# Optimization experiments

Hardware: AMD Instinct MI355X
Metric: run time of the kernel (lower is better)

Reference implementation:

```python
import jax, jax.numpy as jnp
import numpy as np

H = 32          # num attention heads
KVH = 8         # num kv heads
D = 64          # head dim
HID = 2048      # hidden size
MAXB = 1024     # max_bias_length
BASE = 10000.0  # rope theta


def _rope(x, pos):
    # x: (B, S, h, D), pos: (S,) -- GPT-NeoX half-split rotary
    half = D // 2
    inv_freq = 1.0 / (BASE ** (jnp.arange(0, D, 2, dtype=jnp.float32) / D))  # (half,)
    ang = pos[:, None].astype(jnp.float32) * inv_freq                         # (S, half)
    cos = jnp.cos(ang)[None, :, None, :]
    sin = jnp.sin(ang)[None, :, None, :]
    x1, x2 = x[..., :half], x[..., half:]
    return jnp.concatenate([x1 * cos - x2 * sin, x2 * cos + x1 * sin], axis=-1)


def setup_inputs() -> dict:
    key = jax.random.key(0)
    ks = jax.random.split(key, 7)
    B, S = 2, 1024
    hidden_states = jax.random.normal(ks[0], (B, S, HID), dtype=jnp.float32)
    attention_mask = jnp.broadcast_to(
        jnp.tril(jnp.ones((S, S), dtype=jnp.int32))[None, None], (B, 1, S, S))
    # weights stored as (in, out): y = x @ W  (same math as torch Linear)
    Wq = jax.random.normal(ks[1], (HID, H * D), dtype=jnp.float32) * 0.02
    Wk = jax.random.normal(ks[2], (HID, KVH * D), dtype=jnp.float32) * 0.02
    Wv = jax.random.normal(ks[3], (HID, KVH * D), dtype=jnp.float32) * 0.02
    Wo = jax.random.normal(ks[4], (H * D, HID), dtype=jnp.float32) * 0.02
    bias_diag = jax.random.normal(ks[5], (H, MAXB), dtype=jnp.float32) * 0.001
    softmax_offset = jnp.zeros((H,), dtype=jnp.float32)
    return {"hidden_states": hidden_states, "attention_mask": attention_mask,
            "Wq": Wq, "Wk": Wk, "Wv": Wv, "Wo": Wo,
            "bias_diag": bias_diag, "softmax_offset": softmax_offset}


def reference(hidden_states, attention_mask, Wq, Wk, Wv, Wo, bias_diag, softmax_offset):
    B, S, _ = hidden_states.shape
    scaling = D ** (-0.5)
    pos = jnp.arange(S)

    q = (hidden_states @ Wq).reshape(B, S, H, D)
    k = (hidden_states @ Wk).reshape(B, S, KVH, D)
    v = (hidden_states @ Wv).reshape(B, S, KVH, D)

    q = _rope(q, pos)
    k = _rope(k, pos)

    # (B, H, S, D); repeat_kv via repeat on head axis
    q = q.transpose(0, 2, 1, 3)
    k = jnp.repeat(k.transpose(0, 2, 1, 3), H // KVH, axis=1)
    v = jnp.repeat(v.transpose(0, 2, 1, 3), H // KVH, axis=1)

    scores = jnp.einsum('bhqd,bhkd->bhqk', q, k) * scaling

    # learnable diagonal relative-position bias
    rel = pos[:, None] - pos[None, :]                     # (S, S)
    valid = ((rel >= 0) & (rel < MAXB)).astype(scores.dtype)
    idx = jnp.clip(rel, 0, MAXB - 1)
    bias = bias_diag[:, idx] * valid                      # (H, S, S)
    scores = scores + bias[None]

    scores = jnp.where(attention_mask[:, :, :, :S] == 0, -jnp.inf, scores)

    weights = jax.nn.softmax(scores.astype(jnp.float32), axis=-1)

    # adaptive offset subtraction + relu
    offset = jnp.abs(softmax_offset + 1.0)[None, :, None, None]
    num_visible = (pos + 1).astype(jnp.float32)[None, None, :, None]  # along query dim
    weights = jax.nn.relu(weights - offset / num_visible)

    attn_out = jnp.einsum('bhqk,bhkd->bhqd', weights.astype(v.dtype), v)
    attn_out = attn_out.transpose(0, 2, 1, 3).reshape(B, S, H * D)
    return attn_out @ Wo
```

## Files before the change

### kernel.cpp

```cpp
#include <hip/hip_runtime.h>
#include <cstdint>
#include <cstddef>

#define BB   2
#define SS   1024
#define HID  2048
#define HH   32
#define KVHH 8
#define DD   64
#define NQKV 3072
#define QKW  2560

typedef __attribute__((ext_vector_type(8))) short bf16x8;
typedef __attribute__((ext_vector_type(4))) float f32x4;
typedef __attribute__((ext_vector_type(4))) unsigned int u32x4;

__device__ __forceinline__ unsigned short f2bf(float f) {
    unsigned int u = __float_as_uint(f);
    unsigned int r = (u + 0x7fffu + ((u >> 16) & 1u)) >> 16;
    return (unsigned short)r;
}

__device__ __forceinline__ void g2l16(const unsigned short* g, unsigned short* l) {
    __builtin_amdgcn_global_load_lds(
        (__attribute__((address_space(1))) void*)(unsigned short*)g,
        (__attribute__((address_space(3))) void*)l,
        16, 0, 0);
}

__global__ __launch_bounds__(256) void prep(
    const float* __restrict__ hidden,
    const float* __restrict__ Wq, const float* __restrict__ Wk,
    const float* __restrict__ Wv, const float* __restrict__ Wo,
    unsigned short* __restrict__ hidden_bf,
    unsigned short* __restrict__ WqkvT,
    unsigned short* __restrict__ WoT)
{
    const int z   = blockIdx.z;
    const int tid = threadIdx.x;

    if (z == 4) {
        int r0 = blockIdx.y * 64, c0 = blockIdx.x * 64;
        #pragma unroll
        for (int p = 0; p < 4; ++p) {
            int f = tid + p * 256;
            int row = r0 + (f >> 4), c4 = c0 + (f & 15) * 4;
            float4 v = *(const float4*)&hidden[(size_t)row * 2048 + c4];
            ushort4 o;
            o.x = f2bf(v.x); o.y = f2bf(v.y); o.z = f2bf(v.z); o.w = f2bf(v.w);
            *(ushort4*)&hidden_bf[(size_t)row * 2048 + c4] = o;
        }
        return;
    }

    const float* W;
    unsigned short* Wt;
    int N;
    if (z == 0)      { W = Wq; Wt = WqkvT;                        N = 2048; }
    else if (z == 1) { W = Wk; Wt = WqkvT + (size_t)2048 * 2048;  N = 512;  }
    else if (z == 2) { W = Wv; Wt = WqkvT + (size_t)2560 * 2048;  N = 512;  }
    else             { W = Wo; Wt = WoT;                          N = 2048; }
    if (blockIdx.x * 64 >= N) return;

    __shared__ float t[64][68];
    const int n0 = blockIdx.x * 64, k0 = blockIdx.y * 64;
    #pragma unroll
    for (int p = 0; p < 4; ++p) {
        int f = tid + p * 256;
        int row = f >> 4, c4 = (f & 15) * 4;
        float4 v = *(const float4*)&W[(size_t)(k0 + row) * N + n0 + c4];
        t[row][c4 + 0] = v.x; t[row][c4 + 1] = v.y;
        t[row][c4 + 2] = v.z; t[row][c4 + 3] = v.w;
    }
    __syncthreads();
    #pragma unroll
    for (int p = 0; p < 4; ++p) {
        int f = tid + p * 256;
        int nrow = f >> 4, kc4 = (f & 15) * 4;
        ushort4 o;
        o.x = f2bf(t[kc4 + 0][nrow]);
        o.y = f2bf(t[kc4 + 1][nrow]);
        o.z = f2bf(t[kc4 + 2][nrow]);
        o.w = f2bf(t[kc4 + 3][nrow]);
        *(ushort4*)&Wt[(size_t)(n0 + nrow) * 2048 + k0 + kc4] = o;
    }
}

__global__ __launch_bounds__(256) void gemm_qkv_fused(
    const unsigned short* __restrict__ A,
    const unsigned short* __restrict__ Bt,
    unsigned short* __restrict__ qk_bf,
    unsigned short* __restrict__ v_t)
{
    __shared__ __align__(16) char smem[33024];
    short* Asb = (short*)smem;
    short* Bsb = (short*)(smem + 16384);
    float* Ctf = (float*)smem;

    const int tid  = threadIdx.x;
    const int lane = tid & 63;
    const int wave = tid >> 6;
    const int quad = lane >> 4;
    const int l15  = lane & 15;
    const int wm = (wave >> 1) * 64, wn = (wave & 1) * 64;
    const int m0 = blockIdx.y * 128, n0 = blockIdx.x * 128;
    const int K = 2048;

    f32x4 acc[4][4] = {};

    for (int k0 = 0; k0 < K; k0 += 64) {
        #pragma unroll
        for (int p = 0; p < 4; ++p) {
            int ci = tid + p * 256;
            int row = ci >> 3, sc = (ci & 7) ^ (row & 7);
            g2l16(&A[(size_t)(m0 + row) * K + k0 + sc * 8],
                  (unsigned short*)Asb + ci * 8);
        }
        #pragma unroll
        for (int p = 0; p < 4; ++p) {
            int ci = tid + p * 256;
            int row = ci >> 3, sc = (ci & 7) ^ (row & 7);
            g2l16(&Bt[(size_t)(n0 + row) * K + k0 + sc * 8],
                  (unsigned short*)Bsb + ci * 8);
        }
        __syncthreads();

        #pragma unroll
        for (int s = 0; s < 2; ++s) {
            bf16x8 af[4], bfr[4];
            #pragma unroll
            for (int i = 0; i < 4; ++i) {
                int row = wm + i * 16 + l15;
                af[i] = *(const bf16x8*)(Asb + row * 64 +
                        ((((s << 2) | quad) ^ (row & 7)) * 8));
            }
            #pragma unroll
            for (int j = 0; j < 4; ++j) {
                int row = wn + j * 16 + l15;
                bfr[j] = *(const bf16x8*)(Bsb + row * 64 +
                        ((((s << 2) | quad) ^ (row & 7)) * 8));
            }
            #pragma unroll
            for (int i = 0; i < 4; ++i)
                #pragma unroll
                for (int j = 0; j < 4; ++j)
                    acc[i][j] = __builtin_amdgcn_mfma_f32_16x16x32_bf16(
                        af[i], bfr[j], acc[i][j], 0, 0, 0);
        }
        __syncthreads();
    }

    const int bx = blockIdx.x;
    const int b  = m0 >> 10;
    const int s0 = m0 & 1023;
    const int hcg = bx * 128;

    #pragma unroll 1
    for (int ph = 0; ph < 2; ++ph) {
        if (ph) __syncthreads();
        if ((wave >> 1) == ph) {
            #pragma unroll
            for (int i = 0; i < 4; ++i)
                #pragma unroll
                for (int j = 0; j < 4; ++j)
                    #pragma unroll
                    for (int rg = 0; rg < 4; ++rg)
                        Ctf[(i * 16 + quad * 4 + rg) * 129 + wn + j * 16 + l15]
                            = acc[i][j][rg];
        }
        __syncthreads();

        if (bx < 20) {
            const float scale = (bx < 16) ? 0.125f : 1.0f;
            #pragma unroll
            for (int p = 0; p < 4; ++p) {
                int idx = tid + p * 256;
                int row = idx >> 4, hi = (idx >> 3) & 1, t0 = (idx & 7) * 4;
                int s = s0 + ph * 64 + row;
                ushort4 o1, o2;
                #pragma unroll
                for (int k = 0; k < 4; ++k) {
                    int t = t0 + k;
                    float x1 = Ctf[row * 129 + hi * 64 + t];
                    float x2 = Ctf[row * 129 + hi * 64 + t + 32];
                    float inv = __expf(-(float)t * 0.28782313662425572f);
                    float ang = (float)s * inv;
                    float c  = __cosf(ang);
                    float sn = __sinf(ang);
                    ((unsigned short*)&o1)[k] = f2bf((x1 * c - x2 * sn) * scale);
                    ((unsigned short*)&o2)[k] = f2bf((x2 * c + x1 * sn) * scale);
                }
                unsigned short* dst =
                    qk_bf + (size_t)(m0 + ph * 64 + row) * QKW + hcg + hi * 64;
                *(ushort4*)&dst[t0]      = o1;
                *(ushort4*)&dst[t0 + 32] = o2;
            }
        } else {
            const int vb = b * 512 + (bx - 20) * 128;
            #pragma unroll
            for (int p = 0; p < 8; ++p) {
                int idx = tid + p * 256;
                int cc = idx >> 4, srow = (idx & 15) * 4;
                ushort4 o;
                #pragma unroll
                for (int k = 0; k < 4; ++k)
                    ((unsigned short*)&o)[k] = f2bf(Ctf[(srow + k) * 129 + cc]);
                *(ushort4*)&v_t[(size_t)(vb + cc) * 1024 + s0 + ph * 64 + srow] = o;
            }
        }
    }
}

__global__ __launch_bounds__(256) void gemm_bf16_bt(
    const unsigned short* __restrict__ A,
    const unsigned short* __restrict__ Bt,
    float* __restrict__ C, int M, int N, int K)
{
    __shared__ short Asb[128 * 64];
    __shared__ short Bsb[64 * 64];

    const int tid  = threadIdx.x;
    const int lane = tid & 63;
    const int wave = tid >> 6;
    const int quad = lane >> 4;
    const int l15  = lane & 15;
    const int wm = (wave >> 1) * 64, wn = (wave & 1) * 32;
    const int m0 = blockIdx.y * 128, n0 = blockIdx.x * 64;

    f32x4 acc[4][2] = {};

    for (int k0 = 0; k0 < K; k0 += 64) {
        #pragma unroll
        for (int p = 0; p < 4; ++p) {
            int ci = tid + p * 256;
            int row = ci >> 3, sc = (ci & 7) ^ (row & 7);
            g2l16(&A[(size_t)(m0 + row) * K + k0 + sc * 8],
                  (unsigned short*)Asb + ci * 8);
        }
        #pragma unroll
        for (int p = 0; p < 2; ++p) {
            int ci = tid + p * 256;
            int row = ci >> 3, sc = (ci & 7) ^ (row & 7);
            g2l16(&Bt[(size_t)(n0 + row) * K + k0 + sc * 8],
                  (unsigned short*)Bsb + ci * 8);
        }
        __syncthreads();

        #pragma unroll
        for (int s = 0; s < 2; ++s) {
            bf16x8 af[4], bfr[2];
            #pragma unroll
            for (int i = 0; i < 4; ++i) {
                int row = wm + i * 16 + l15;
                af[i] = *(const bf16x8*)(Asb + row * 64 +
                        ((((s << 2) | quad) ^ (row & 7)) * 8));
            }
            #pragma unroll
            for (int j = 0; j < 2; ++j) {
                int row = wn + j * 16 + l15;
                bfr[j] = *(const bf16x8*)(Bsb + row * 64 +
                        ((((s << 2) | quad) ^ (row & 7)) * 8));
            }
            #pragma unroll
            for (int i = 0; i < 4; ++i)
                #pragma unroll
                for (int j = 0; j < 2; ++j)
                    acc[i][j] = __builtin_amdgcn_mfma_f32_16x16x32_bf16(
                        af[i], bfr[j], acc[i][j], 0, 0, 0);
        }
        __syncthreads();
    }

    #pragma unroll
    for (int i = 0; i < 4; ++i) {
        int grow = m0 + wm + i * 16 + quad * 4;
        #pragma unroll
        for (int j = 0; j < 2; ++j) {
            int gcol = n0 + wn + j * 16 + l15;
            #pragma unroll
            for (int rg = 0; rg < 4; ++rg)
                C[(size_t)(grow + rg) * N + gcol] = acc[i][j][rg];
        }
    }
}

__global__ __launch_bounds__(512, 4) void attn_mfma(
    const unsigned short* __restrict__ qk_bf,
    const unsigned short* __restrict__ v_t,
    const float* __restrict__ bias_diag,
    const float* __restrict__ soff,
    unsigned short* __restrict__ AO)
{
    const int id = (int)blockIdx.x;
    const int h  = id & 31;
    const int b  = (id >> 5) & 1;
    const int pi = id >> 6;
    const int kh = h >> 2;
    const int tid  = threadIdx.x;
    const int lane = tid & 63;
    const int wave = tid >> 6;
    const int grp  = wave >> 2;
    const int w4   = wave & 3;
    const int gt   = tid & 255;
    const int quad = lane >> 4;
    const int l15  = lane & 15;

    __shared__ short Ks[2][2][4096];
    __shared__ short Vs[2][2][4096];
    __shared__ float bd_s[1024];
    __shared__ float red[2][64];

    for (int i = tid; i < 1024; i += 512) bd_s[i] = bias_diag[h * 1024 + i];

    const unsigned short* Kg = qk_bf + (size_t)(b * SS) * QKW + 2048 + kh * 64;
    const unsigned short* Vg = v_t + (size_t)(b * 512 + kh * 64) * SS;

    short* KsG = &Ks[grp][0][0];
    short* VsG = &Vs[grp][0][0];
    float* Fred = (float*)&Ks[1][0][0];

#define STAGE_K(j, buf) do {                                                  \
    _Pragma("unroll")                                                         \
    for (int p = 0; p < 2; ++p) {                                             \
        int ci = gt + p * 256;                                                \
        int row_ = ci >> 3;                                                   \
        int sc_  = (ci & 7) ^ (row_ & 7);                                     \
        g2l16(Kg + (size_t)((j) * 64 + row_) * QKW + sc_ * 8,                 \
              (unsigned short*)(KsG + (buf) * 4096 + ci * 8));                \
    } } while (0)

#define STAGE_V(j, buf) do {                                                  \
    _Pragma("unroll")                                                         \
    for (int p = 0; p < 2; ++p) {                                             \
        int ci = gt + p * 256;                                                \
        int row_ = ci >> 3;                                                   \
        int sc_  = (ci & 7) ^ (row_ & 7);                                     \
        g2l16(Vg + (size_t)row_ * SS + (j) * 64 + sc_ * 8,                    \
              (unsigned short*)(VsG + (buf) * 4096 + ci * 8));                \
    } } while (0)

    #pragma unroll 1
    for (int half = 0; half < 2; ++half) {
        const int qt = half ? pi : 15 - pi;
        const int q0 = qt * 64;
        const int nI = (qt + 2) >> 1;
        const int qrow = q0 + w4 * 16 + l15;

        const unsigned short* Qg =
            qk_bf + (size_t)(b * SS + q0 + w4 * 16) * QKW + h * 64;
        bf16x8 qf0 = *(const bf16x8*)(Qg + (size_t)l15 * QKW + quad * 8);
        bf16x8 qf1 = *(const bf16x8*)(Qg + (size_t)l15 * QKW + 32 + quad * 8);

        float lpa[4] = {0.f, 0.f, 0.f, 0.f};
        if (grp <= qt) STAGE_K(grp, 0);
        __syncthreads();
        int cur = 0;
        for (int i = 0; i < nI; ++i) {
            const int j = 2 * i + grp;
            if (j + 2 <= qt) STAGE_K(j + 2, cur ^ 1);
            if (j <= qt) {
                const short* Kb = KsG + cur * 4096;
                const bool diag = (j == qt);
                f32x4 acc[4] = {};
                #pragma unroll
                for (int nb = 0; nb < 4; ++nb) {
                    if (diag && nb > w4) continue;
                    int row = nb * 16 + l15, sw = row & 7;
                    bf16x8 a0 = *(const bf16x8*)(Kb + row * 64 + ((quad ^ sw) * 8));
                    bf16x8 a1 = *(const bf16x8*)(Kb + row * 64 + (((quad + 4) ^ sw) * 8));
                    acc[nb] = __builtin_amdgcn_mfma_f32_16x16x32_bf16(a0, qf0, acc[nb], 0, 0, 0);
                    acc[nb] = __builtin_amdgcn_mfma_f32_16x16x32_bf16(a1, qf1, acc[nb], 0, 0, 0);
                }
                if (!diag) {
                    #pragma unroll
                    for (int nb = 0; nb < 4; ++nb) {
                        int rel0 = qrow - (j * 64 + nb * 16 + quad * 4);
                        #pragma unroll
                        for (int r = 0; r < 4; ++r)
                            lpa[r] += __expf(acc[nb][r] + bd_s[rel0 - r]);
                    }
                } else {
                    #pragma unroll
                    for (int nb = 0; nb < 4; ++nb) {
                        if (nb > w4) continue;
                        #pragma unroll
                        for (int r = 0; r < 4; ++r) {
                            int rel = qrow - (j * 64 + nb * 16 + quad * 4 + r);
                            if (rel >= 0) lpa[r] += __expf(acc[nb][r] + bd_s[rel]);
                        }
                    }
                }
            }
            __syncthreads();
            cur ^= 1;
        }

        float lp = (lpa[0] + lpa[1]) + (lpa[2] + lpa[3]);
        lp += __shfl_xor(lp, 16, 64);
        lp += __shfl_xor(lp, 32, 64);
        if (quad == 0) red[grp][w4 * 16 + l15] = lp;
        __syncthreads();
        lp = red[0][w4 * 16 + l15] + red[1][w4 * 16 + l15];
        const float invl = 1.f / lp;
        const float cl   = fabsf(soff[h] + 1.f) / (float)(qrow + 1) * lp;

        f32x4 oacc[4] = {};
        if (grp <= qt) { STAGE_K(grp, 0); STAGE_V(grp, 0); }
        __syncthreads();
        cur = 0;
        for (int i = 0; i < nI; ++i) {
            const int j = 2 * i + grp;
            if (j + 2 <= qt) { STAGE_K(j + 2, cur ^ 1); STAGE_V(j + 2, cur ^ 1); }
            if (j <= qt) {
                const short* Kb = KsG + cur * 4096;
                const short* Vb = VsG + cur * 4096;
                const bool diag = (j == qt);

                f32x4 acc[4] = {};
                #pragma unroll
                for (int nb = 0; nb < 4; ++nb) {
                    if (diag && nb > w4) continue;
                    int row = nb * 16 + l15, sw = row & 7;
                    bf16x8 a0 = *(const bf16x8*)(Kb + row * 64 + ((quad ^ sw) * 8));
                    bf16x8 a1 = *(const bf16x8*)(Kb + row * 64 + (((quad + 4) ^ sw) * 8));
                    acc[nb] = __builtin_amdgcn_mfma_f32_16x16x32_bf16(a0, qf0, acc[nb], 0, 0, 0);
                    acc[nb] = __builtin_amdgcn_mfma_f32_16x16x32_bf16(a1, qf1, acc[nb], 0, 0, 0);
                }

                unsigned int pk[4][2];
                if (!diag) {
                    #pragma unroll
                    for (int nb = 0; nb < 4; ++nb) {
                        float w[4];
                        int rel0 = qrow - (j * 64 + nb * 16 + quad * 4);
                        #pragma unroll
                        for (int r = 0; r < 4; ++r)
                            w[r] = fmaxf(__expf(acc[nb][r] + bd_s[rel0 - r]) - cl, 0.f);
                        asm("v_cvt_pk_bf16_f32 %0, %1, %2" : "=v"(pk[nb][0]) : "v"(w[0]), "v"(w[1]));
                        asm("v_cvt_pk_bf16_f32 %0, %1, %2" : "=v"(pk[nb][1]) : "v"(w[2]), "v"(w[3]));
                    }
                } else {
                    #pragma unroll
                    for (int nb = 0; nb < 4; ++nb) {
                        float w[4];
                        #pragma unroll
                        for (int r = 0; r < 4; ++r) {
                            int rel = qrow - (j * 64 + nb * 16 + quad * 4 + r);
                            float e = 0.f;
                            if (rel >= 0)
                                e = fmaxf(__expf(acc[nb][r] + bd_s[rel]) - cl, 0.f);
                            w[r] = e;
                        }
                        asm("v_cvt_pk_bf16_f32 %0, %1, %2" : "=v"(pk[nb][0]) : "v"(w[0]), "v"(w[1]));
                        asm("v_cvt_pk_bf16_f32 %0, %1, %2" : "=v"(pk[nb][1]) : "v"(w[2]), "v"(w[3]));
                    }
                }
                unsigned int ppk[4][2];
                #pragma unroll
                for (int nb = 0; nb < 4; ++nb) {
                    ppk[nb][0] = __shfl_xor(pk[nb][0], 16, 64);
                    ppk[nb][1] = __shfl_xor(pk[nb][1], 16, 64);
                }

                const bool oddq = quad & 1;
                const int  cv   = ((quad & 1) << 1) | (quad >> 1);
                #pragma unroll
                for (int s = 0; s < 2; ++s) {
                    if (diag && s == 1 && w4 < 2) continue;
                    unsigned int w0 = oddq ? ppk[2 * s + 1][0] : pk[2 * s][0];
                    unsigned int w1 = oddq ? ppk[2 * s + 1][1] : pk[2 * s][1];
                    unsigned int w2 = oddq ? pk[2 * s + 1][0]  : ppk[2 * s][0];
                    unsigned int w3 = oddq ? pk[2 * s + 1][1]  : ppk[2 * s][1];
                    u32x4 t; t[0] = w0; t[1] = w1; t[2] = w2; t[3] = w3;
                    bf16x8 pf = __builtin_bit_cast(bf16x8, t);
                    #pragma unroll
                    for (int nd = 0; nd < 4; ++nd) {
                        int rowv = nd * 16 + l15, swv = rowv & 7;
                        bf16x8 vf = *(const bf16x8*)(Vb + rowv * 64 + (((cv + 4 * s) ^ swv) * 8));
                        oacc[nd] = __builtin_amdgcn_mfma_f32_16x16x32_bf16(pf, vf, oacc[nd], 0, 0, 0);
                    }
                }
            }
            __syncthreads();
            cur ^= 1;
        }

        if (grp == 1) {
            #pragma unroll
            for (int nd = 0; nd < 4; ++nd)
                #pragma unroll
                for (int r = 0; r < 4; ++r)
                    Fred[(w4 * 16 + quad * 4 + r) * 64 + nd * 16 + l15] = oacc[nd][r];
        }
        __syncthreads();
        if (grp == 0) {
            float invl_r[4];
            #pragma unroll
            for (int r = 0; r < 4; ++r)
                invl_r[r] = __shfl(invl, quad * 4 + r, 64);
            unsigned short* aop =
                AO + (size_t)(b * SS + q0 + w4 * 16 + quad * 4) * 2048 + h * 64 + l15;
            #pragma unroll
            for (int nd = 0; nd < 4; ++nd)
                #pragma unroll
                for (int r = 0; r < 4; ++r) {
                    float o = (oacc[nd][r] +
                               Fred[(w4 * 16 + quad * 4 + r) * 64 + nd * 16 + l15])
                              * invl_r[r];
                    aop[(size_t)r * 2048 + nd * 16] = f2bf(o);
                }
        }
        __syncthreads();
    }
#undef STAGE_K
#undef STAGE_V
}

extern "C" void kernel_launch(void* const* d_in, const int* in_sizes, int n_in,
                              void* d_out, int out_size, void* d_ws, size_t ws_size,
                              hipStream_t stream)
{
    const float* hidden    = (const float*)d_in[0];
    const float* Wq        = (const float*)d_in[2];
    const float* Wk        = (const float*)d_in[3];
    const float* Wv        = (const float*)d_in[4];
    const float* Wo        = (const float*)d_in[5];
    const float* bias_diag = (const float*)d_in[6];
    const float* soff      = (const float*)d_in[7];
    float* out = (float*)d_out;

    char* wsb = (char*)d_ws;
    unsigned short* hidden_bf = (unsigned short*)wsb;
    unsigned short* WqkvT     = (unsigned short*)(wsb + (size_t)8388608);
    unsigned short* AO_bf     = (unsigned short*)(wsb + (size_t)12582912);
    unsigned short* WoT       = (unsigned short*)(wsb + (size_t)20971520);
    unsigned short* qk_bf     = (unsigned short*)(wsb + (size_t)29360128);
    unsigned short* v_t       = (unsigned short*)(wsb + (size_t)29360128 + (size_t)2048 * 2560 * 2);

    prep<<<dim3(32, 32, 5), dim3(256), 0, stream>>>(
        hidden, Wq, Wk, Wv, Wo, hidden_bf, WqkvT, WoT);

    gemm_qkv_fused<<<dim3(24, 16), dim3(256), 0, stream>>>(
        hidden_bf, WqkvT, qk_bf, v_t);

    attn_mfma<<<dim3(512), dim3(512), 0, stream>>>(
        qk_bf, v_t, bias_diag, soff, AO_bf);

    gemm_bf16_bt<<<dim3(2048 / 64, 2048 / 128), dim3(256), 0, stream>>>(
        AO_bf, WoT, out, 2048, 2048, 2048);
}
```

Measured before the change: 226.1 us.

## Double-buffer LDS in QKV and output GEMMs, shrink QKV tile to 128x64

Both GEMMs now use a two-stage LDS ring: the global-to-LDS load for the next K slice is issued before the MFMAs on the current slice, so load latency overlaps compute and one barrier per iteration is removed. The QKV GEMM tile drops from 128x128 to 128x64, doubling the grid to 768 blocks for better CU fill on the 256-CU device. The epilogue RoPE and V-transpose are remapped to 64-column tiles. The cost is more LDS per block (48KB), fewer accumulators per wave, and more redundant A-tile loads.

Measured after the change: 203.2 us. 10.2% less time.

```diff
diff --git a/kernel.cpp b/kernel.cpp
--- a/kernel.cpp
+++ b/kernel.cpp
@@ -92,132 +92,8 @@
     unsigned short* __restrict__ qk_bf,
     unsigned short* __restrict__ v_t)
 {
-    __shared__ __align__(16) char smem[33024];
-    short* Asb = (short*)smem;
-    short* Bsb = (short*)(smem + 16384);
+    __shared__ __align__(16) char smem[49152];
     float* Ctf = (float*)smem;
-
-    const int tid  = threadIdx.x;
-    const int lane = tid & 63;
-    const int wave = tid >> 6;
-    const int quad = lane >> 4;
-    const int l15  = lane & 15;
-    const int wm = (wave >> 1) * 64, wn = (wave & 1) * 64;
-    const int m0 = blockIdx.y * 128, n0 = blockIdx.x * 128;
-    const int K = 2048;
-
-    f32x4 acc[4][4] = {};
-
-    for (int k0 = 0; k0 < K; k0 += 64) {
-        #pragma unroll
-        for (int p = 0; p < 4; ++p) {
-            int ci = tid + p * 256;
-            int row = ci >> 3, sc = (ci & 7) ^ (row & 7);
-            g2l16(&A[(size_t)(m0 + row) * K + k0 + sc * 8],
-                  (unsigned short*)Asb + ci * 8);
-        }
-        #pragma unroll
-        for (int p = 0; p < 4; ++p) {
-            int ci = tid + p * 256;
-            int row = ci >> 3, sc = (ci & 7) ^ (row & 7);
-            g2l16(&Bt[(size_t)(n0 + row) * K + k0 + sc * 8],
-                  (unsigned short*)Bsb + ci * 8);
-        }
-        __syncthreads();
-
-        #pragma unroll
-        for (int s = 0; s < 2; ++s) {
-            bf16x8 af[4], bfr[4];
-            #pragma unroll
-            for (int i = 0; i < 4; ++i) {
-                int row = wm + i * 16 + l15;
-                af[i] = *(const bf16x8*)(Asb + row * 64 +
-                        ((((s << 2) | quad) ^ (row & 7)) * 8));
-            }
-            #pragma unroll
-            for (int j = 0; j < 4; ++j) {
-                int row = wn + j * 16 + l15;
-                bfr[j] = *(const bf16x8*)(Bsb + row * 64 +
-                        ((((s << 2) | quad) ^ (row & 7)) * 8));
-            }
-            #pragma unroll
-            for (int i = 0; i < 4; ++i)
-                #pragma unroll
-                for (int j = 0; j < 4; ++j)
-                    acc[i][j] = __builtin_amdgcn_mfma_f32_16x16x32_bf16(
-                        af[i], bfr[j], acc[i][j], 0, 0, 0);
-        }
-        __syncthreads();
-    }
-
-    const int bx = blockIdx.x;
-    const int b  = m0 >> 10;
-    const int s0 = m0 & 1023;
-    const int hcg = bx * 128;
-
-    #pragma unroll 1
-    for (int ph = 0; ph < 2; ++ph) {
-        if (ph) __syncthreads();
-        if ((wave >> 1) == ph) {
-            #pragma unroll
-            for (int i = 0; i < 4; ++i)
-                #pragma unroll
-                for (int j = 0; j < 4; ++j)
-                    #pragma unroll
-                    for (int rg = 0; rg < 4; ++rg)
-                        Ctf[(i * 16 + quad * 4 + rg) * 129 + wn + j * 16 + l15]
-                            = acc[i][j][rg];
-        }
-        __syncthreads();
-
-        if (bx < 20) {
-            const float scale = (bx < 16) ? 0.125f : 1.0f;
-            #pragma unroll
-            for (int p = 0; p < 4; ++p) {
-                int idx = tid + p * 256;
-                int row = idx >> 4, hi = (idx >> 3) & 1, t0 = (idx & 7) * 4;
-                int s = s0 + ph * 64 + row;
-                ushort4 o1, o2;
-                #pragma unroll
-                for (int k = 0; k < 4; ++k) {
-                    int t = t0 + k;
-                    float x1 = Ctf[row * 129 + hi * 64 + t];
-                    float x2 = Ctf[row * 129 + hi * 64 + t + 32];
-                    float inv = __expf(-(float)t * 0.28782313662425572f);
-                    float ang = (float)s * inv;
-                    float c  = __cosf(ang);
-                    float sn = __sinf(ang);
-                    ((unsigned short*)&o1)[k] = f2bf((x1 * c - x2 * sn) * scale);
-                    ((unsigned short*)&o2)[k] = f2bf((x2 * c + x1 * sn) * scale);
-                }
-                unsigned short* dst =
-                    qk_bf + (size_t)(m0 + ph * 64 + row) * QKW + hcg + hi * 64;
-                *(ushort4*)&dst[t0]      = o1;
-                *(ushort4*)&dst[t0 + 32] = o2;
-            }
-        } else {
-            const int vb = b * 512 + (bx - 20) * 128;
-            #pragma unroll
-            for (int p = 0; p < 8; ++p) {
-                int idx = tid + p * 256;
-                int cc = idx >> 4, srow = (idx & 15) * 4;
-                ushort4 o;
-                #pragma unroll
-                for (int k = 0; k < 4; ++k)
-                    ((unsigned short*)&o)[k] = f2bf(Ctf[(srow + k) * 129 + cc]);
-                *(ushort4*)&v_t[(size_t)(vb + cc) * 1024 + s0 + ph * 64 + srow] = o;
-            }
-        }
-    }
-}
-
-__global__ __launch_bounds__(256) void gemm_bf16_bt(
-    const unsigned short* __restrict__ A,
-    const unsigned short* __restrict__ Bt,
-    float* __restrict__ C, int M, int N, int K)
-{
-    __shared__ short Asb[128 * 64];
-    __shared__ short Bsb[64 * 64];
 
     const int tid  = threadIdx.x;
     const int lane = tid & 63;
@@ -226,25 +102,33 @@
     const int l15  = lane & 15;
     const int wm = (wave >> 1) * 64, wn = (wave & 1) * 32;
     const int m0 = blockIdx.y * 128, n0 = blockIdx.x * 64;
+    const int K = 2048;
 
     f32x4 acc[4][2] = {};
 
+#define STAGE_Q(k0s, buf) do {                                                \
+    unsigned short* Ad = (unsigned short*)(smem + (buf) * 24576);             \
+    unsigned short* Bd = (unsigned short*)(smem + (buf) * 24576 + 16384);     \
+    _Pragma("unroll")                                                         \
+    for (int p = 0; p < 4; ++p) {                                             \
+        int ci = tid + p * 256;                                               \
+        int row_ = ci >> 3, sc_ = (ci & 7) ^ (row_ & 7);                      \
+        g2l16(&A[(size_t)(m0 + row_) * K + (k0s) + sc_ * 8], Ad + ci * 8);    \
+    }                                                                         \
+    _Pragma("unroll")                                                         \
+    for (int p = 0; p < 2; ++p) {                                             \
+        int ci = tid + p * 256;                                               \
+        int row_ = ci >> 3, sc_ = (ci & 7) ^ (row_ & 7);                      \
+        g2l16(&Bt[(size_t)(n0 + row_) * K + (k0s) + sc_ * 8], Bd + ci * 8);   \
+    } } while (0)
+
+    STAGE_Q(0, 0);
+    __syncthreads();
+    int cur = 0;
     for (int k0 = 0; k0 < K; k0 += 64) {
-        #pragma unroll
-        for (int p = 0; p < 4; ++p) {
-            int ci = tid + p * 256;
-            int row = ci >> 3, sc = (ci & 7) ^ (row & 7);
-            g2l16(&A[(size_t)(m0 + row) * K + k0 + sc * 8],
-                  (unsigned short*)Asb + ci * 8);
-        }
-        #pragma unroll
-        for (int p = 0; p < 2; ++p) {
-            int ci = tid + p * 256;
-            int row = ci >> 3, sc = (ci & 7) ^ (row & 7);
-            g2l16(&Bt[(size_t)(n0 + row) * K + k0 + sc * 8],
-                  (unsigned short*)Bsb + ci * 8);
-        }
-        __syncthreads();
+        if (k0 + 64 < K) STAGE_Q(k0 + 64, cur ^ 1);
+        const short* Ab = (const short*)(smem + cur * 24576);
+        const short* Bb = (const short*)(smem + cur * 24576 + 16384);
 
         #pragma unroll
         for (int s = 0; s < 2; ++s) {
@@ -252,13 +136,13 @@
             #pragma unroll
             for (int i = 0; i < 4; ++i) {
                 int row = wm + i * 16 + l15;
-                af[i] = *(const bf16x8*)(Asb + row * 64 +
+                af[i] = *(const bf16x8*)(Ab + row * 64 +
                         ((((s << 2) | quad) ^ (row & 7)) * 8));
             }
             #pragma unroll
             for (int j = 0; j < 2; ++j) {
                 int row = wn + j * 16 + l15;
-                bfr[j] = *(const bf16x8*)(Bsb + row * 64 +
+                bfr[j] = *(const bf16x8*)(Bb + row * 64 +
                         ((((s << 2) | quad) ^ (row & 7)) * 8));
             }
             #pragma unroll
@@ -269,6 +153,129 @@
                         af[i], bfr[j], acc[i][j], 0, 0, 0);
         }
         __syncthreads();
+        cur ^= 1;
+    }
+
+    #pragma unroll
+    for (int i = 0; i < 4; ++i)
+        #pragma unroll
+        for (int j = 0; j < 2; ++j)
+            #pragma unroll
+            for (int rg = 0; rg < 4; ++rg)
+                Ctf[(wm + i * 16 + quad * 4 + rg) * 65 + wn + j * 16 + l15]
+                    = acc[i][j][rg];
+    __syncthreads();
+
+    const int bx = blockIdx.x;
+    const int b  = m0 >> 10;
+    const int s0 = m0 & 1023;
+
+    if (bx < 40) {
+        const int hc = bx * 64;
+        const float scale = (bx < 32) ? 0.125f : 1.0f;
+        #pragma unroll
+        for (int p = 0; p < 4; ++p) {
+            int idx = tid + p * 256;
+            int row = idx >> 3, t0 = (idx & 7) * 4;
+            int s = s0 + row;
+            ushort4 o1, o2;
+            #pragma unroll
+            for (int k = 0; k < 4; ++k) {
+                int t = t0 + k;
+                float x1 = Ctf[row * 65 + t];
+                float x2 = Ctf[row * 65 + t + 32];
+                float inv = __expf(-(float)t * 0.28782313662425572f);
+                float ang = (float)s * inv;
+                float c  = __cosf(ang);
+                float sn = __sinf(ang);
+                ((unsigned short*)&o1)[k] = f2bf((x1 * c - x2 * sn) * scale);
+                ((unsigned short*)&o2)[k] = f2bf((x2 * c + x1 * sn) * scale);
+            }
+            unsigned short* dst = qk_bf + (size_t)(m0 + row) * QKW + hc;
+            *(ushort4*)&dst[t0]      = o1;
+            *(ushort4*)&dst[t0 + 32] = o2;
+        }
+    } else {
+        const int vb = b * 512 + (bx - 40) * 64;
+        #pragma unroll
+        for (int p = 0; p < 8; ++p) {
+            int idx = tid + p * 256;
+            int c = idx >> 5, srow = (idx & 31) * 4;
+            ushort4 o;
+            #pragma unroll
+            for (int k = 0; k < 4; ++k)
+                ((unsigned short*)&o)[k] = f2bf(Ctf[(srow + k) * 65 + c]);
+            *(ushort4*)&v_t[(size_t)(vb + c) * 1024 + s0 + srow] = o;
+        }
+    }
+#undef STAGE_Q
+}
+
+__global__ __launch_bounds__(256) void gemm_bf16_bt(
+    const unsigned short* __restrict__ A,
+    const unsigned short* __restrict__ Bt,
+    float* __restrict__ C, int M, int N, int K)
+{
+    __shared__ __align__(16) char smem[49152];
+
+    const int tid  = threadIdx.x;
+    const int lane = tid & 63;
+    const int wave = tid >> 6;
+    const int quad = lane >> 4;
+    const int l15  = lane & 15;
+    const int wm = (wave >> 1) * 64, wn = (wave & 1) * 32;
+    const int m0 = blockIdx.y * 128, n0 = blockIdx.x * 64;
+
+    f32x4 acc[4][2] = {};
+
+#define STAGE_O(k0s, buf) do {                                                \
+    unsigned short* Ad = (unsigned short*)(smem + (buf) * 24576);             \
+    unsigned short* Bd = (unsigned short*)(smem + (buf) * 24576 + 16384);     \
+    _Pragma("unroll")                                                         \
+    for (int p = 0; p < 4; ++p) {                                             \
+        int ci = tid + p * 256;                                               \
+        int row_ = ci >> 3, sc_ = (ci & 7) ^ (row_ & 7);                      \
+        g2l16(&A[(size_t)(m0 + row_) * K + (k0s) + sc_ * 8], Ad + ci * 8);    \
+    }                                                                         \
+    _Pragma("unroll")                                                         \
+    for (int p = 0; p < 2; ++p) {                                             \
+        int ci = tid + p * 256;                                               \
+        int row_ = ci >> 3, sc_ = (ci & 7) ^ (row_ & 7);                      \
+        g2l16(&Bt[(size_t)(n0 + row_) * K + (k0s) + sc_ * 8], Bd + ci * 8);   \
+    } } while (0)
+
+    STAGE_O(0, 0);
+    __syncthreads();
+    int cur = 0;
+    for (int k0 = 0; k0 < K; k0 += 64) {
+        if (k0 + 64 < K) STAGE_O(k0 + 64, cur ^ 1);
+        const short* Ab = (const short*)(smem + cur * 24576);
+        const short* Bb = (const short*)(smem + cur * 24576 + 16384);
+
+        #pragma unroll
+        for (int s = 0; s < 2; ++s) {
+            bf16x8 af[4], bfr[2];
+            #pragma unroll
+            for (int i = 0; i < 4; ++i) {
+                int row = wm + i * 16 + l15;
+                af[i] = *(const bf16x8*)(Ab + row * 64 +
+                        ((((s << 2) | quad) ^ (row & 7)) * 8));
+            }
+            #pragma unroll
+            for (int j = 0; j < 2; ++j) {
+                int row = wn + j * 16 + l15;
+                bfr[j] = *(const bf16x8*)(Bb + row * 64 +
+                        ((((s << 2) | quad) ^ (row & 7)) * 8));
+            }
+            #pragma unroll
+            for (int i = 0; i < 4; ++i)
+                #pragma unroll
+                for (int j = 0; j < 2; ++j)
+                    acc[i][j] = __builtin_amdgcn_mfma_f32_16x16x32_bf16(
+                        af[i], bfr[j], acc[i][j], 0, 0, 0);
+        }
+        __syncthreads();
+        cur ^= 1;
     }
 
     #pragma unroll
@@ -282,6 +289,7 @@
                 C[(size_t)(grow + rg) * N + gcol] = acc[i][j][rg];
         }
     }
+#undef STAGE_O
 }
 
 __global__ __launch_bounds__(512, 4) void attn_mfma(
@@ -540,7 +548,7 @@
     prep<<<dim3(32, 32, 5), dim3(256), 0, stream>>>(
         hidden, Wq, Wk, Wv, Wo, hidden_bf, WqkvT, WoT);
 
-    gemm_qkv_fused<<<dim3(24, 16), dim3(256), 0, stream>>>(
+    gemm_qkv_fused<<<dim3(48, 16), dim3(256), 0, stream>>>(
         hidden_bf, WqkvT, qk_bf, v_t);
 
     attn_mfma<<<dim3(512), dim3(512), 0, stream>>>(
```
